# Optimization experiments

Hardware: AMD Instinct MI355X
Metric: run time of the kernel (lower is better)

Reference implementation:

```python
import jax, jax.numpy as jnp
import numpy as np

N = 100000
E = 1600000
IN, HID, OUT = 128, 32, 32


def gcn_conv(x, ei, ew, W, b, n):
    # PyG GCNConv: symmetric norm with self-loops, edge_attr as edge weight
    h = x @ W                                  # [n, d_out]
    row, col = ei[0], ei[1]
    loop = jnp.arange(n)
    row = jnp.concatenate([row, loop])
    col = jnp.concatenate([col, loop])
    ew = jnp.concatenate([ew, jnp.ones((n,), ew.dtype)])
    deg = jax.ops.segment_sum(ew, col, num_segments=n)
    dinv = jnp.where(deg > 0, jax.lax.rsqrt(deg), 0.0)
    norm = dinv[row] * ew * dinv[col]          # [E+n]
    out = jax.ops.segment_sum(norm[:, None] * h[row], col, num_segments=n)
    return out + b


def setup_inputs() -> dict:
    key = jax.random.key(0)
    ks = jax.random.split(key, 24)
    inp = {}
    for i in range(3):
        inp[f"x{i+1}"] = jax.random.normal(ks[i], (N, IN), jnp.float32)
        inp[f"ei{i+1}"] = jax.random.randint(ks[3 + i], (2, E), 0, N, jnp.int64)
        inp[f"ea{i+1}"] = jax.random.uniform(ks[6 + i], (E,), jnp.float32)
        inp[f"W{i+1}"] = jax.random.normal(ks[9 + i], (IN, HID), jnp.float32) * (IN ** -0.5)
        inp[f"b{i+1}"] = jnp.zeros((HID,), jnp.float32)
        inp[f"Wo{i+1}"] = jax.random.normal(ks[12 + i], (HID, OUT), jnp.float32) * (HID ** -0.5)
        inp[f"bo{i+1}"] = jnp.zeros((OUT,), jnp.float32)
    inp["att_w"] = jax.random.normal(ks[15], (HID, 1), jnp.float32) * (HID ** -0.5)
    return inp


def reference(x1, x2, x3, ei1, ei2, ei3, ea1, ea2, ea3,
              W1, W2, W3, b1, b2, b3,
              Wo1, Wo2, Wo3, bo1, bo2, bo3, att_w):
    xs = [x1, x2, x3]
    eis = [ei1, ei2, ei3]
    eas = [ea1, ea2, ea3]
    Ws = [W1, W2, W3]
    bs = [b1, b2, b3]
    Wos = [Wo1, Wo2, Wo3]
    bos = [bo1, bo2, bo3]

    embs, coefs = [], []
    for x, ei, ea, W, b in zip(xs, eis, eas, Ws, bs):
        e = jax.nn.relu(gcn_conv(x, ei, ea, W, b, N))   # [N, HID]; dropout is eval no-op
        embs.append(e)
        coefs.append(jnp.exp(jax.nn.leaky_relu(e @ att_w)))  # [N, 1]
    coef_sum = coefs[0] + coefs[1] + coefs[2]
    weights = [c / coef_sum for c in coefs]
    h = sum(w * e for w, e in zip(weights, embs))       # [N, HID]

    out = sum(gcn_conv(h, ei, ea, Wo, bo, N)
              for ei, ea, Wo, bo in zip(eis, eas, Wos, bos))
    return (out, weights[0], weights[1], weights[2])
```

## Files before the change

### kernel.cpp

```cpp
#include <hip/hip_runtime.h>
#include <hip/hip_fp16.h>

typedef unsigned short u16;
typedef unsigned int   u32;

#define N_NODES 100000
#define N_EDGES 1600000
#define IN_DIM  128
#define HID_DIM 32
#define OUT_DIM 32

#define BK   128
#define NBC  782
#define NBT  (3 * NBC)

#define PB    384
#define BINB  1024
#define CHUNK 12500
#define SC_N  (NBT * PB)
#define SC_CHUNK 2048
#define SC_G  ((SC_N + SC_CHUNK - 1) / SC_CHUNK)
#define CAP  3072
#define GN8  ((N_NODES * 8) / 256)


__global__ void binhist_kernel(const int* __restrict__ ei0, const int* __restrict__ ei1,
                               const int* __restrict__ ei2, int* __restrict__ hist_t) {
    __shared__ int hloc[NBT];
    for (int i = threadIdx.x; i < NBT; i += blockDim.x) hloc[i] = 0;
    __syncthreads();
    int b = blockIdx.x;
    int beg = b * CHUNK, end = beg + CHUNK;
    for (int e = beg + threadIdx.x; e < end; e += blockDim.x) {
        int c = (e >= 2 * N_EDGES) ? 2 : (e >= N_EDGES ? 1 : 0);
        const int* ei = (c == 0) ? ei0 : (c == 1) ? ei1 : ei2;
        int col = ei[N_EDGES + (e - c * N_EDGES)];
        atomicAdd(&hloc[c * NBC + (col >> 7)], 1);
    }
    __syncthreads();
    for (int g = threadIdx.x; g < NBT; g += blockDim.x)
        hist_t[g * PB + b] = hloc[g];
}


__global__ void scan1_kernel(const int* __restrict__ counts, int* __restrict__ rp1,
                             int* __restrict__ blocksum) {
    __shared__ int wsum[4];
    int tid = threadIdx.x;
    int base = blockIdx.x * SC_CHUNK + tid * 8;
    int vals[8];
    int tsum = 0;
    if (base < SC_N) {
        int4 v0 = *(const int4*)(counts + base);
        int4 v1 = *(const int4*)(counts + base + 4);
        vals[0] = v0.x; vals[1] = v0.y; vals[2] = v0.z; vals[3] = v0.w;
        vals[4] = v1.x; vals[5] = v1.y; vals[6] = v1.z; vals[7] = v1.w;
#pragma unroll
        for (int k = 0; k < 8; k++) tsum += vals[k];
    } else {
#pragma unroll
        for (int k = 0; k < 8; k++) vals[k] = 0;
    }
    int lane = tid & 63, wave = tid >> 6;
    int x = tsum;
    for (int d = 1; d < 64; d <<= 1) {
        int t = __shfl_up(x, d, 64);
        if (lane >= d) x += t;
    }
    if (lane == 63) wsum[wave] = x;
    __syncthreads();
    int woff = 0;
    for (int w = 0; w < wave; w++) woff += wsum[w];
    int run = woff + x - tsum;
    if (base < SC_N) {
#pragma unroll
        for (int k = 0; k < 8; k++) {
            run += vals[k];
            rp1[base + k + 1] = run;
        }
    }
    if (tid == blockDim.x - 1) blocksum[blockIdx.x] = woff + x;
}

__global__ void scan2_kernel(int* __restrict__ blocksum, int n) {
    __shared__ int wsum[4];
    int tid = threadIdx.x;
    int lane = tid & 63, wave = tid >> 6;
    int carry = 0;
    for (int base = 0; base < n; base += 256) {
        int i = base + tid;
        int v = (i < n) ? blocksum[i] : 0;
        int x = v;
        for (int d = 1; d < 64; d <<= 1) {
            int t = __shfl_up(x, d, 64);
            if (lane >= d) x += t;
        }
        if (lane == 63) wsum[wave] = x;
        __syncthreads();
        int woff = 0;
        for (int w = 0; w < wave; w++) woff += wsum[w];
        int total = wsum[0] + wsum[1] + wsum[2] + wsum[3];
        if (i < n) blocksum[i] = carry + woff + x - v;
        carry += total;
        __syncthreads();
    }
}

__global__ void scan3_kernel(int* __restrict__ rp1, const int* __restrict__ blocksum) {
    int i = blockIdx.x * blockDim.x + threadIdx.x;
    if (i < SC_N) rp1[i + 1] += blocksum[i / SC_CHUNK];
    if (i == 0) rp1[0] = 0;
}


__global__ void binscatter_kernel(const int* __restrict__ ei0, const int* __restrict__ ei1,
                                  const int* __restrict__ ei2,
                                  const float* __restrict__ ea0, const float* __restrict__ ea1,
                                  const float* __restrict__ ea2,
                                  const int* __restrict__ ofs, int2* __restrict__ stg) {
    __shared__ int base_l[NBT];
    int b = blockIdx.x;
    for (int g = threadIdx.x; g < NBT; g += blockDim.x) base_l[g] = ofs[g * PB + b];
    __syncthreads();
    int beg = b * CHUNK, end = beg + CHUNK;
    for (int e = beg + threadIdx.x; e < end; e += blockDim.x) {
        int c = (e >= 2 * N_EDGES) ? 2 : (e >= N_EDGES ? 1 : 0);
        int le = e - c * N_EDGES;
        const int* ei = (c == 0) ? ei0 : (c == 1) ? ei1 : ei2;
        const float* ea = (c == 0) ? ea0 : (c == 1) ? ea1 : ea2;
        int row = ei[le];
        int col = ei[N_EDGES + le];
        int g = c * NBC + (col >> 7);
        int slot = atomicAdd(&base_l[g], 1);
        stg[slot] = make_int2(row | ((col & 127) << 17), __float_as_int(ea[le]));
    }
}


__global__ void bucket_sort_kernel(int2* __restrict__ stg, const int* __restrict__ ofs,
                                   float* __restrict__ dinv, int* __restrict__ row_ptr) {
    __shared__ int2 buf[CAP];
    __shared__ int hist[BK];
    __shared__ float deg[BK];
    __shared__ float dl[BK];
    __shared__ int pref[BK];
    __shared__ int fill[BK];
    __shared__ int wtot;
    int tid = threadIdx.x;
    int g = blockIdx.x;
    int c = g / NBC;
    int colBase = (g % NBC) << 7;
    if (tid < BK) { hist[tid] = 0; deg[tid] = 1.0f; fill[tid] = 0; }
    __syncthreads();
    int beg = ofs[g * PB];
    int end = (g == NBT - 1) ? 3 * N_EDGES : ofs[(g + 1) * PB];
    int cnt = end - beg;
    if (cnt > CAP) cnt = CAP;
    for (int i = tid; i < cnt; i += blockDim.x) {
        int2 p = stg[beg + i];
        buf[i] = p;
        int cl = (p.x >> 17) & 127;
        atomicAdd(&hist[cl], 1);
        atomicAdd(&deg[cl], __int_as_float(p.y));
    }
    __syncthreads();
    int x = 0;
    if (tid < BK) {
        x = hist[tid];
        int lane = tid & 63;
        for (int d = 1; d < 64; d <<= 1) {
            int t = __shfl_up(x, d, 64);
            if (lane >= d) x += t;
        }
        if (tid == 63) wtot = x;
    }
    __syncthreads();
    if (tid < BK) {
        int incl = (tid >= 64) ? x + wtot : x;
        pref[tid] = incl - hist[tid];
        dl[tid] = rsqrtf(deg[tid]);
    }
    __syncthreads();
    for (int i = tid; i < cnt; i += blockDim.x) {
        int2 p = buf[i];
        int cl = (p.x >> 17) & 127;
        int r = atomicAdd(&fill[cl], 1);
        float v = __int_as_float(p.y) * dl[cl];
        stg[beg + pref[cl] + r] = make_int2(p.x, __float_as_int(v));
    }
    int col = colBase + tid;
    if (tid < BK && col < N_NODES) {
        dinv[(size_t)c * N_NODES + col] = dl[tid];
        row_ptr[(size_t)c * N_NODES + col] = beg + pref[tid];
    }
    if (g == NBT - 1 && tid == 0) row_ptr[3 * N_NODES] = 3 * N_EDGES;
}


__device__ inline u32 pack_half2(float a, float b) {
    __half2 h = __floats2half2_rn(a, b);
    union { __half2 h; u32 u; } cv; cv.h = h;
    return cv.u;
}

__device__ inline float2 unpack_half2(u32 u) {
    union { u32 u; __half2 h; } cv; cv.u = u;
    return __half22float2(cv.h);
}


__global__ void matmul_in3_kernel(const float* __restrict__ x0, const float* __restrict__ x1,
                                  const float* __restrict__ x2,
                                  const float* __restrict__ W0, const float* __restrict__ W1,
                                  const float* __restrict__ W2,
                                  const float* __restrict__ dinv,
                                  u16* __restrict__ h3) {
    __shared__ float Ws[IN_DIM * HID_DIM];
    int c = blockIdx.x / GN8;
    int lb = blockIdx.x % GN8;
    const float* x = (c == 0) ? x0 : (c == 1) ? x1 : x2;
    const float* W = (c == 0) ? W0 : (c == 1) ? W1 : W2;
    for (int i = threadIdx.x; i < IN_DIM * HID_DIM; i += blockDim.x) Ws[i] = W[i];
    __syncthreads();
    int gid = lb * blockDim.x + threadIdx.x;
    int v = gid >> 3;
    int t = gid & 7;
    const float* xr = x + (size_t)v * IN_DIM;
    float a0 = 0.f, a1 = 0.f, a2 = 0.f, a3 = 0.f;
#pragma unroll
    for (int j = 0; j < IN_DIM; j += 4) {
        float4 xv = *(const float4*)(xr + j);
        const float* wb = &Ws[j * HID_DIM + 4 * t];
        float4 w0 = *(const float4*)(wb);
        float4 w1 = *(const float4*)(wb + 32);
        float4 w2 = *(const float4*)(wb + 64);
        float4 w3 = *(const float4*)(wb + 96);
        a0 += xv.x * w0.x + xv.y * w1.x + xv.z * w2.x + xv.w * w3.x;
        a1 += xv.x * w0.y + xv.y * w1.y + xv.z * w2.y + xv.w * w3.y;
        a2 += xv.x * w0.z + xv.y * w1.z + xv.z * w2.z + xv.w * w3.z;
        a3 += xv.x * w0.w + xv.y * w1.w + xv.z * w2.w + xv.w * w3.w;
    }
    float s = dinv[(size_t)c * N_NODES + v];
    uint2 pk = make_uint2(pack_half2(a0 * s, a1 * s), pack_half2(a2 * s, a3 * s));
    *(uint2*)(h3 + ((size_t)c * N_NODES + v) * HID_DIM + 4 * t) = pk;
}


__global__ void matmul_hid3_kernel(const float* __restrict__ hmix,
                                   const float* __restrict__ Wo0, const float* __restrict__ Wo1,
                                   const float* __restrict__ Wo2,
                                   const float* __restrict__ dinv,
                                   u16* __restrict__ h23) {
    __shared__ float Ws[HID_DIM * OUT_DIM];
    int c = blockIdx.x / GN8;
    int lb = blockIdx.x % GN8;
    const float* Wo = (c == 0) ? Wo0 : (c == 1) ? Wo1 : Wo2;
    for (int i = threadIdx.x; i < HID_DIM * OUT_DIM; i += blockDim.x) Ws[i] = Wo[i];
    __syncthreads();
    int gid = lb * blockDim.x + threadIdx.x;
    int v = gid >> 3;
    int t = gid & 7;
    const float* hr = hmix + (size_t)v * HID_DIM;
    float a0 = 0.f, a1 = 0.f, a2 = 0.f, a3 = 0.f;
#pragma unroll
    for (int j = 0; j < HID_DIM; j += 4) {
        float4 hv = *(const float4*)(hr + j);
        const float* wb = &Ws[j * OUT_DIM + 4 * t];
        float4 w0 = *(const float4*)(wb);
        float4 w1 = *(const float4*)(wb + 32);
        float4 w2 = *(const float4*)(wb + 64);
        float4 w3 = *(const float4*)(wb + 96);
        a0 += hv.x * w0.x + hv.y * w1.x + hv.z * w2.x + hv.w * w3.x;
        a1 += hv.x * w0.y + hv.y * w1.y + hv.z * w2.y + hv.w * w3.y;
        a2 += hv.x * w0.z + hv.y * w1.z + hv.z * w2.z + hv.w * w3.z;
        a3 += hv.x * w0.w + hv.y * w1.w + hv.z * w2.w + hv.w * w3.w;
    }
    float s = dinv[(size_t)c * N_NODES + v];
    uint2 pk = make_uint2(pack_half2(a0 * s, a1 * s), pack_half2(a2 * s, a3 * s));
    *(uint2*)(h23 + ((size_t)c * N_NODES + v) * OUT_DIM + 4 * t) = pk;
}


__global__ void gather_combine_kernel(const int* __restrict__ row_ptr,
                                      const int2* __restrict__ csr,
                                      const u16* __restrict__ h3,
                                      const float* __restrict__ dinv,
                                      const float* __restrict__ b0,
                                      const float* __restrict__ b1,
                                      const float* __restrict__ b2,
                                      const float* __restrict__ att_w,
                                      float* __restrict__ hmix,
                                      float* __restrict__ wout) {
    int gid = blockIdx.x * blockDim.x + threadIdx.x;
    int v = gid >> 3;
    int t = gid & 7;
    float4 wv = *(const float4*)(att_w + t * 4);
    float e[3][4];
    float coef[3];
#pragma unroll
    for (int c = 0; c < 3; c++) {
        const u16* h = h3 + (size_t)c * N_NODES * HID_DIM;
        const float* bb = (c == 0) ? b0 : (c == 1) ? b1 : b2;
        int beg = row_ptr[c * N_NODES + v], end = row_ptr[c * N_NODES + v + 1];
        float a0 = 0.f, a1 = 0.f, a2 = 0.f, a3 = 0.f;
        for (int ee = beg; ee < end; ee++) {
            int2 p = csr[ee];
            int row = p.x & 0x1FFFF;
            float val = __int_as_float(p.y);
            uint2 u = *(const uint2*)(h + (size_t)row * HID_DIM + 4 * t);
            float2 f0 = unpack_half2(u.x);
            float2 f1 = unpack_half2(u.y);
            a0 += val * f0.x; a1 += val * f0.y; a2 += val * f1.x; a3 += val * f1.y;
        }
        float s = dinv[(size_t)c * N_NODES + v];
        uint2 u = *(const uint2*)(h + (size_t)v * HID_DIM + 4 * t);
        float2 f0 = unpack_half2(u.x);
        float2 f1 = unpack_half2(u.y);
        float4 bv = *(const float4*)(bb + t * 4);
        e[c][0] = fmaxf(a0 + s * f0.x + bv.x, 0.f);
        e[c][1] = fmaxf(a1 + s * f0.y + bv.y, 0.f);
        e[c][2] = fmaxf(a2 + s * f1.x + bv.z, 0.f);
        e[c][3] = fmaxf(a3 + s * f1.y + bv.w, 0.f);
        float dot = e[c][0] * wv.x + e[c][1] * wv.y + e[c][2] * wv.z + e[c][3] * wv.w;
        dot += __shfl_xor(dot, 1, 64);
        dot += __shfl_xor(dot, 2, 64);
        dot += __shfl_xor(dot, 4, 64);
        float lr = (dot > 0.0f) ? dot : 0.01f * dot;
        coef[c] = expf(lr);
    }
    float inv = 1.0f / (coef[0] + coef[1] + coef[2]);
    float w0 = coef[0] * inv, w1 = coef[1] * inv, w2 = coef[2] * inv;
    if (t == 0) {
        wout[v] = w0;
        wout[N_NODES + v] = w1;
        wout[2 * N_NODES + v] = w2;
    }
    float4 r;
    r.x = w0 * e[0][0] + w1 * e[1][0] + w2 * e[2][0];
    r.y = w0 * e[0][1] + w1 * e[1][1] + w2 * e[2][1];
    r.z = w0 * e[0][2] + w1 * e[1][2] + w2 * e[2][2];
    r.w = w0 * e[0][3] + w1 * e[1][3] + w2 * e[2][3];
    *(float4*)(hmix + (size_t)v * HID_DIM + t * 4) = r;
}


__global__ void gather_out_kernel(const int* __restrict__ row_ptr,
                                  const int2* __restrict__ csr,
                                  const u16* __restrict__ h23,
                                  const float* __restrict__ dinv,
                                  const float* __restrict__ bo0,
                                  const float* __restrict__ bo1,
                                  const float* __restrict__ bo2,
                                  float* __restrict__ out) {
    int gid = blockIdx.x * blockDim.x + threadIdx.x;
    int v = gid >> 3;
    int t = gid & 7;
    float4 b0 = *(const float4*)(bo0 + t * 4);
    float4 b1 = *(const float4*)(bo1 + t * 4);
    float4 b2 = *(const float4*)(bo2 + t * 4);
    float a0 = b0.x + b1.x + b2.x;
    float a1 = b0.y + b1.y + b2.y;
    float a2 = b0.z + b1.z + b2.z;
    float a3 = b0.w + b1.w + b2.w;
#pragma unroll
    for (int c = 0; c < 3; c++) {
        const u16* h2 = h23 + (size_t)c * N_NODES * OUT_DIM;
        int beg = row_ptr[c * N_NODES + v], end = row_ptr[c * N_NODES + v + 1];
        for (int ee = beg; ee < end; ee++) {
            int2 p = csr[ee];
            int row = p.x & 0x1FFFF;
            float val = __int_as_float(p.y);
            uint2 u = *(const uint2*)(h2 + (size_t)row * OUT_DIM + 4 * t);
            float2 f0 = unpack_half2(u.x);
            float2 f1 = unpack_half2(u.y);
            a0 += val * f0.x; a1 += val * f0.y; a2 += val * f1.x; a3 += val * f1.y;
        }
        float s = dinv[(size_t)c * N_NODES + v];
        uint2 u = *(const uint2*)(h2 + (size_t)v * OUT_DIM + 4 * t);
        float2 f0 = unpack_half2(u.x);
        float2 f1 = unpack_half2(u.y);
        a0 += s * f0.x; a1 += s * f0.y; a2 += s * f1.x; a3 += s * f1.y;
    }
    float4 ov; ov.x = a0; ov.y = a1; ov.z = a2; ov.w = a3;
    *(float4*)(out + (size_t)v * OUT_DIM + t * 4) = ov;
}


extern "C" void kernel_launch(void* const* d_in, const int* in_sizes, int n_in,
                              void* d_out, int out_size, void* d_ws, size_t ws_size,
                              hipStream_t stream) {
    const float* x[3];  const int* ei[3];  const float* ea[3];
    const float* W[3];  const float* b[3]; const float* Wo[3]; const float* bo[3];
    for (int c = 0; c < 3; c++) {
        x[c]  = (const float*)d_in[7 * c + 0];
        ei[c] = (const int*)  d_in[7 * c + 1];
        ea[c] = (const float*)d_in[7 * c + 2];
        W[c]  = (const float*)d_in[7 * c + 3];
        b[c]  = (const float*)d_in[7 * c + 4];
        Wo[c] = (const float*)d_in[7 * c + 5];
        bo[c] = (const float*)d_in[7 * c + 6];
    }
    const float* att_w = (const float*)d_in[21];
    float* out = (float*)d_out;
    float* wout = out + (size_t)N_NODES * OUT_DIM;

    int*   wsb      = (int*)d_ws;
    float* dinv     = (float*)wsb;
    int*   row_ptr  = wsb + 3 * N_NODES;
    int*   blocksum = row_ptr + 3 * N_NODES + 4;
    size_t stg_off  = (size_t)(3 * N_NODES + 3 * N_NODES + 4 + 512);
    stg_off = (stg_off + 3) & ~(size_t)3;
    int2*  stg      = (int2*)(wsb + stg_off);
    u16*   hA       = (u16*)(stg + 3 * (size_t)N_EDGES);
    int*   hist_t   = (int*)hA;
    int*   ofs      = hist_t + SC_N;
    float* hmix     = (float*)(hA + 3 * (size_t)N_NODES * HID_DIM);

    const int B = 256;

    binhist_kernel<<<PB, BINB, 0, stream>>>(ei[0], ei[1], ei[2], hist_t);
    scan1_kernel<<<SC_G, B, 0, stream>>>(hist_t, ofs, blocksum);
    scan2_kernel<<<1, B, 0, stream>>>(blocksum, SC_G);
    scan3_kernel<<<(SC_N + B - 1) / B, B, 0, stream>>>(ofs, blocksum);
    binscatter_kernel<<<PB, BINB, 0, stream>>>(ei[0], ei[1], ei[2], ea[0], ea[1], ea[2],
                                               ofs, stg);
    bucket_sort_kernel<<<NBT, B, 0, stream>>>(stg, ofs, dinv, row_ptr);

    matmul_in3_kernel<<<3 * GN8, B, 0, stream>>>(x[0], x[1], x[2], W[0], W[1], W[2],
                                                 dinv, hA);
    gather_combine_kernel<<<GN8, B, 0, stream>>>(row_ptr, stg, hA, dinv,
                                                 b[0], b[1], b[2], att_w, hmix, wout);

    matmul_hid3_kernel<<<3 * GN8, B, 0, stream>>>(hmix, Wo[0], Wo[1], Wo[2], dinv, hA);
    gather_out_kernel<<<GN8, B, 0, stream>>>(row_ptr, stg, hA, dinv,
                                             bo[0], bo[1], bo[2], out);
}
```

Measured before the change: 687.6 us.

## Pack CSR entries into 32 bits, widen gather threads, drop scan3 pass

Bucket sort now writes a separate 4-byte CSR entry per edge holding the 17-bit row index and a 15-bit half-precision normalized weight (sign bit dropped), instead of an 8-byte int2. This halves the index traffic in both gather kernels. The gather kernels switch from 8 to 4 threads per node, each loading 16-byte half vectors, which cuts shuffle steps and redundant CSR reads. The scan3 fixup kernel is removed: block carries are added on the fly wherever offsets are read, and the binning partition count changes from 384 to 256 blocks. The cost is reduced edge-weight precision and fewer threads in flight for the gathers.

```diff
diff --git a/kernel.cpp b/kernel.cpp
--- a/kernel.cpp
+++ b/kernel.cpp
@@ -14,14 +14,19 @@
 #define NBC  782
 #define NBT  (3 * NBC)
 
-#define PB    384
+#define PB    256
 #define BINB  1024
-#define CHUNK 12500
+#define CHUNK 18750
 #define SC_N  (NBT * PB)
 #define SC_CHUNK 2048
 #define SC_G  ((SC_N + SC_CHUNK - 1) / SC_CHUNK)
 #define CAP  3072
 #define GN8  ((N_NODES * 8) / 256)
+#define GN4  ((N_NODES * 4 + 255) / 256)
+
+__device__ inline int ofs_at(const int* __restrict__ rp1, const int* __restrict__ bs, int m) {
+    return m ? rp1[m] + bs[(m - 1) >> 11] : 0;
+}
 
 
 __global__ void binhist_kernel(const int* __restrict__ ei0, const int* __restrict__ ei1,
@@ -80,6 +85,7 @@
         }
     }
     if (tid == blockDim.x - 1) blocksum[blockIdx.x] = woff + x;
+    if (blockIdx.x == 0 && tid == 0) rp1[0] = 0;
 }
 
 __global__ void scan2_kernel(int* __restrict__ blocksum, int n) {
@@ -106,21 +112,17 @@
     }
 }
 
-__global__ void scan3_kernel(int* __restrict__ rp1, const int* __restrict__ blocksum) {
-    int i = blockIdx.x * blockDim.x + threadIdx.x;
-    if (i < SC_N) rp1[i + 1] += blocksum[i / SC_CHUNK];
-    if (i == 0) rp1[0] = 0;
-}
-
 
 __global__ void binscatter_kernel(const int* __restrict__ ei0, const int* __restrict__ ei1,
                                   const int* __restrict__ ei2,
                                   const float* __restrict__ ea0, const float* __restrict__ ea1,
                                   const float* __restrict__ ea2,
-                                  const int* __restrict__ ofs, int2* __restrict__ stg) {
+                                  const int* __restrict__ rp1, const int* __restrict__ bsum,
+                                  int2* __restrict__ stg) {
     __shared__ int base_l[NBT];
     int b = blockIdx.x;
-    for (int g = threadIdx.x; g < NBT; g += blockDim.x) base_l[g] = ofs[g * PB + b];
+    for (int g = threadIdx.x; g < NBT; g += blockDim.x)
+        base_l[g] = ofs_at(rp1, bsum, g * PB + b);
     __syncthreads();
     int beg = b * CHUNK, end = beg + CHUNK;
     for (int e = beg + threadIdx.x; e < end; e += blockDim.x) {
@@ -137,7 +139,9 @@
 }
 
 
-__global__ void bucket_sort_kernel(int2* __restrict__ stg, const int* __restrict__ ofs,
+__global__ void bucket_sort_kernel(const int2* __restrict__ stg, const int* __restrict__ rp1,
+                                   const int* __restrict__ bsum,
+                                   u32* __restrict__ csr,
                                    float* __restrict__ dinv, int* __restrict__ row_ptr) {
     __shared__ int2 buf[CAP];
     __shared__ int hist[BK];
@@ -152,8 +156,8 @@
     int colBase = (g % NBC) << 7;
     if (tid < BK) { hist[tid] = 0; deg[tid] = 1.0f; fill[tid] = 0; }
     __syncthreads();
-    int beg = ofs[g * PB];
-    int end = (g == NBT - 1) ? 3 * N_EDGES : ofs[(g + 1) * PB];
+    int beg = ofs_at(rp1, bsum, g * PB);
+    int end = (g == NBT - 1) ? 3 * N_EDGES : ofs_at(rp1, bsum, (g + 1) * PB);
     int cnt = end - beg;
     if (cnt > CAP) cnt = CAP;
     for (int i = tid; i < cnt; i += blockDim.x) {
@@ -186,7 +190,9 @@
         int cl = (p.x >> 17) & 127;
         int r = atomicAdd(&fill[cl], 1);
         float v = __int_as_float(p.y) * dl[cl];
-        stg[beg + pref[cl] + r] = make_int2(p.x, __float_as_int(v));
+        __half h = __float2half(v);
+        u32 hb = (u32)(*(u16*)&h) & 0x7FFF;
+        csr[beg + pref[cl] + r] = (u32)(p.x & 0x1FFFF) | (hb << 17);
     }
     int col = colBase + tid;
     if (tid < BK && col < N_NODES) {
@@ -206,6 +212,10 @@
 __device__ inline float2 unpack_half2(u32 u) {
     union { u32 u; __half2 h; } cv; cv.u = u;
     return __half22float2(cv.h);
+}
+
+__device__ inline float val15(u32 meta) {
+    return unpack_half2(meta >> 17).x;
 }
 
 
@@ -282,7 +292,7 @@
 
 
 __global__ void gather_combine_kernel(const int* __restrict__ row_ptr,
-                                      const int2* __restrict__ csr,
+                                      const u32* __restrict__ csr,
                                       const u16* __restrict__ h3,
                                       const float* __restrict__ dinv,
                                       const float* __restrict__ b0,
@@ -292,39 +302,49 @@
                                       float* __restrict__ hmix,
                                       float* __restrict__ wout) {
     int gid = blockIdx.x * blockDim.x + threadIdx.x;
-    int v = gid >> 3;
-    int t = gid & 7;
-    float4 wv = *(const float4*)(att_w + t * 4);
-    float e[3][4];
+    int v = gid >> 2;
+    int t = gid & 3;
+    if (v >= N_NODES) return;
+    float4 wv0 = *(const float4*)(att_w + t * 8);
+    float4 wv1 = *(const float4*)(att_w + t * 8 + 4);
+    float e[3][8];
     float coef[3];
 #pragma unroll
     for (int c = 0; c < 3; c++) {
         const u16* h = h3 + (size_t)c * N_NODES * HID_DIM;
         const float* bb = (c == 0) ? b0 : (c == 1) ? b1 : b2;
         int beg = row_ptr[c * N_NODES + v], end = row_ptr[c * N_NODES + v + 1];
-        float a0 = 0.f, a1 = 0.f, a2 = 0.f, a3 = 0.f;
+        float a[8];
+#pragma unroll
+        for (int k = 0; k < 8; k++) a[k] = 0.f;
         for (int ee = beg; ee < end; ee++) {
-            int2 p = csr[ee];
-            int row = p.x & 0x1FFFF;
-            float val = __int_as_float(p.y);
-            uint2 u = *(const uint2*)(h + (size_t)row * HID_DIM + 4 * t);
-            float2 f0 = unpack_half2(u.x);
-            float2 f1 = unpack_half2(u.y);
-            a0 += val * f0.x; a1 += val * f0.y; a2 += val * f1.x; a3 += val * f1.y;
+            u32 m = csr[ee];
+            int row = m & 0x1FFFF;
+            float val = val15(m);
+            uint4 u = *(const uint4*)(h + (size_t)row * HID_DIM + 8 * t);
+            float2 f0 = unpack_half2(u.x), f1 = unpack_half2(u.y);
+            float2 f2 = unpack_half2(u.z), f3 = unpack_half2(u.w);
+            a[0] += val * f0.x; a[1] += val * f0.y; a[2] += val * f1.x; a[3] += val * f1.y;
+            a[4] += val * f2.x; a[5] += val * f2.y; a[6] += val * f3.x; a[7] += val * f3.y;
         }
         float s = dinv[(size_t)c * N_NODES + v];
-        uint2 u = *(const uint2*)(h + (size_t)v * HID_DIM + 4 * t);
-        float2 f0 = unpack_half2(u.x);
-        float2 f1 = unpack_half2(u.y);
-        float4 bv = *(const float4*)(bb + t * 4);
-        e[c][0] = fmaxf(a0 + s * f0.x + bv.x, 0.f);
-        e[c][1] = fmaxf(a1 + s * f0.y + bv.y, 0.f);
-        e[c][2] = fmaxf(a2 + s * f1.x + bv.z, 0.f);
-        e[c][3] = fmaxf(a3 + s * f1.y + bv.w, 0.f);
-        float dot = e[c][0] * wv.x + e[c][1] * wv.y + e[c][2] * wv.z + e[c][3] * wv.w;
+        uint4 u = *(const uint4*)(h + (size_t)v * HID_DIM + 8 * t);
+        float2 f0 = unpack_half2(u.x), f1 = unpack_half2(u.y);
+        float2 f2 = unpack_half2(u.z), f3 = unpack_half2(u.w);
+        float4 bv0 = *(const float4*)(bb + t * 8);
+        float4 bv1 = *(const float4*)(bb + t * 8 + 4);
+        e[c][0] = fmaxf(a[0] + s * f0.x + bv0.x, 0.f);
+        e[c][1] = fmaxf(a[1] + s * f0.y + bv0.y, 0.f);
+        e[c][2] = fmaxf(a[2] + s * f1.x + bv0.z, 0.f);
+        e[c][3] = fmaxf(a[3] + s * f1.y + bv0.w, 0.f);
+        e[c][4] = fmaxf(a[4] + s * f2.x + bv1.x, 0.f);
+        e[c][5] = fmaxf(a[5] + s * f2.y + bv1.y, 0.f);
+        e[c][6] = fmaxf(a[6] + s * f3.x + bv1.z, 0.f);
+        e[c][7] = fmaxf(a[7] + s * f3.y + bv1.w, 0.f);
+        float dot = e[c][0] * wv0.x + e[c][1] * wv0.y + e[c][2] * wv0.z + e[c][3] * wv0.w
+                  + e[c][4] * wv1.x + e[c][5] * wv1.y + e[c][6] * wv1.z + e[c][7] * wv1.w;
         dot += __shfl_xor(dot, 1, 64);
         dot += __shfl_xor(dot, 2, 64);
-        dot += __shfl_xor(dot, 4, 64);
         float lr = (dot > 0.0f) ? dot : 0.01f * dot;
         coef[c] = expf(lr);
     }
@@ -335,17 +355,22 @@
         wout[N_NODES + v] = w1;
         wout[2 * N_NODES + v] = w2;
     }
-    float4 r;
-    r.x = w0 * e[0][0] + w1 * e[1][0] + w2 * e[2][0];
-    r.y = w0 * e[0][1] + w1 * e[1][1] + w2 * e[2][1];
-    r.z = w0 * e[0][2] + w1 * e[1][2] + w2 * e[2][2];
-    r.w = w0 * e[0][3] + w1 * e[1][3] + w2 * e[2][3];
-    *(float4*)(hmix + (size_t)v * HID_DIM + t * 4) = r;
+    float4 r0, r1;
+    r0.x = w0 * e[0][0] + w1 * e[1][0] + w2 * e[2][0];
+    r0.y = w0 * e[0][1] + w1 * e[1][1] + w2 * e[2][1];
+    r0.z = w0 * e[0][2] + w1 * e[1][2] + w2 * e[2][2];
+    r0.w = w0 * e[0][3] + w1 * e[1][3] + w2 * e[2][3];
+    r1.x = w0 * e[0][4] + w1 * e[1][4] + w2 * e[2][4];
+    r1.y = w0 * e[0][5] + w1 * e[1][5] + w2 * e[2][5];
+    r1.z = w0 * e[0][6] + w1 * e[1][6] + w2 * e[2][6];
+    r1.w = w0 * e[0][7] + w1 * e[1][7] + w2 * e[2][7];
+    *(float4*)(hmix + (size_t)v * HID_DIM + t * 8) = r0;
+    *(float4*)(hmix + (size_t)v * HID_DIM + t * 8 + 4) = r1;
 }
 
 
 __global__ void gather_out_kernel(const int* __restrict__ row_ptr,
-                                  const int2* __restrict__ csr,
+                                  const u32* __restrict__ csr,
                                   const u16* __restrict__ h23,
                                   const float* __restrict__ dinv,
                                   const float* __restrict__ bo0,
@@ -353,36 +378,46 @@
                                   const float* __restrict__ bo2,
                                   float* __restrict__ out) {
     int gid = blockIdx.x * blockDim.x + threadIdx.x;
-    int v = gid >> 3;
-    int t = gid & 7;
-    float4 b0 = *(const float4*)(bo0 + t * 4);
-    float4 b1 = *(const float4*)(bo1 + t * 4);
-    float4 b2 = *(const float4*)(bo2 + t * 4);
-    float a0 = b0.x + b1.x + b2.x;
-    float a1 = b0.y + b1.y + b2.y;
-    float a2 = b0.z + b1.z + b2.z;
-    float a3 = b0.w + b1.w + b2.w;
+    int v = gid >> 2;
+    int t = gid & 3;
+    if (v >= N_NODES) return;
+    float4 p0 = *(const float4*)(bo0 + t * 8);
+    float4 p1 = *(const float4*)(bo0 + t * 8 + 4);
+    float4 q0 = *(const float4*)(bo1 + t * 8);
+    float4 q1 = *(const float4*)(bo1 + t * 8 + 4);
+    float4 s0 = *(const float4*)(bo2 + t * 8);
+    float4 s1 = *(const float4*)(bo2 + t * 8 + 4);
+    float a[8];
+    a[0] = p0.x + q0.x + s0.x; a[1] = p0.y + q0.y + s0.y;
+    a[2] = p0.z + q0.z + s0.z; a[3] = p0.w + q0.w + s0.w;
+    a[4] = p1.x + q1.x + s1.x; a[5] = p1.y + q1.y + s1.y;
+    a[6] = p1.z + q1.z + s1.z; a[7] = p1.w + q1.w + s1.w;
 #pragma unroll
     for (int c = 0; c < 3; c++) {
         const u16* h2 = h23 + (size_t)c * N_NODES * OUT_DIM;
         int beg = row_ptr[c * N_NODES + v], end = row_ptr[c * N_NODES + v + 1];
         for (int ee = beg; ee < end; ee++) {
-            int2 p = csr[ee];
-            int row = p.x & 0x1FFFF;
-            float val = __int_as_float(p.y);
-            uint2 u = *(const uint2*)(h2 + (size_t)row * OUT_DIM + 4 * t);
-            float2 f0 = unpack_half2(u.x);
-            float2 f1 = unpack_half2(u.y);
-            a0 += val * f0.x; a1 += val * f0.y; a2 += val * f1.x; a3 += val * f1.y;
+            u32 m = csr[ee];
+            int row = m & 0x1FFFF;
+            float val = val15(m);
+            uint4 u = *(const uint4*)(h2 + (size_t)row * OUT_DIM + 8 * t);
+            float2 f0 = unpack_half2(u.x), f1 = unpack_half2(u.y);
+            float2 f2 = unpack_half2(u.z), f3 = unpack_half2(u.w);
+            a[0] += val * f0.x; a[1] += val * f0.y; a[2] += val * f1.x; a[3] += val * f1.y;
+            a[4] += val * f2.x; a[5] += val * f2.y; a[6] += val * f3.x; a[7] += val * f3.y;
         }
         float s = dinv[(size_t)c * N_NODES + v];
-        uint2 u = *(const uint2*)(h2 + (size_t)v * OUT_DIM + 4 * t);
-        float2 f0 = unpack_half2(u.x);
-        float2 f1 = unpack_half2(u.y);
-        a0 += s * f0.x; a1 += s * f0.y; a2 += s * f1.x; a3 += s * f1.y;
-    }
-    float4 ov; ov.x = a0; ov.y = a1; ov.z = a2; ov.w = a3;
-    *(float4*)(out + (size_t)v * OUT_DIM + t * 4) = ov;
+        uint4 u = *(const uint4*)(h2 + (size_t)v * OUT_DIM + 8 * t);
+        float2 f0 = unpack_half2(u.x), f1 = unpack_half2(u.y);
+        float2 f2 = unpack_half2(u.z), f3 = unpack_half2(u.w);
+        a[0] += s * f0.x; a[1] += s * f0.y; a[2] += s * f1.x; a[3] += s * f1.y;
+        a[4] += s * f2.x; a[5] += s * f2.y; a[6] += s * f3.x; a[7] += s * f3.y;
+    }
+    float4 o0, o1;
+    o0.x = a[0]; o0.y = a[1]; o0.z = a[2]; o0.w = a[3];
+    o1.x = a[4]; o1.y = a[5]; o1.z = a[6]; o1.w = a[7];
+    *(float4*)(out + (size_t)v * OUT_DIM + t * 8) = o0;
+    *(float4*)(out + (size_t)v * OUT_DIM + t * 8 + 4) = o1;
 }
 
 
@@ -411,27 +446,27 @@
     size_t stg_off  = (size_t)(3 * N_NODES + 3 * N_NODES + 4 + 512);
     stg_off = (stg_off + 3) & ~(size_t)3;
     int2*  stg      = (int2*)(wsb + stg_off);
-    u16*   hA       = (u16*)(stg + 3 * (size_t)N_EDGES);
+    u32*   csr      = (u32*)(stg + 3 * (size_t)N_EDGES);
+    u16*   hA       = (u16*)(csr + 3 * (size_t)N_EDGES);
     int*   hist_t   = (int*)hA;
-    int*   ofs      = hist_t + SC_N;
+    int*   rp1      = hist_t + SC_N;
     float* hmix     = (float*)(hA + 3 * (size_t)N_NODES * HID_DIM);
 
     const int B = 256;
 
     binhist_kernel<<<PB, BINB, 0, stream>>>(ei[0], ei[1], ei[2], hist_t);
-    scan1_kernel<<<SC_G, B, 0, stream>>>(hist_t, ofs, blocksum);
+    scan1_kernel<<<SC_G, B, 0, stream>>>(hist_t, rp1, blocksum);
     scan2_kernel<<<1, B, 0, stream>>>(blocksum, SC_G);
-    scan3_kernel<<<(SC_N + B - 1) / B, B, 0, stream>>>(ofs, blocksum);
     binscatter_kernel<<<PB, BINB, 0, stream>>>(ei[0], ei[1], ei[2], ea[0], ea[1], ea[2],
-                                               ofs, stg);
-    bucket_sort_kernel<<<NBT, B, 0, stream>>>(stg, ofs, dinv, row_ptr);
+                                               rp1, blocksum, stg);
+    bucket_sort_kernel<<<NBT, B, 0, stream>>>(stg, rp1, blocksum, csr, dinv, row_ptr);
 
     matmul_in3_kernel<<<3 * GN8, B, 0, stream>>>(x[0], x[1], x[2], W[0], W[1], W[2],
                                                  dinv, hA);
-    gather_combine_kernel<<<GN8, B, 0, stream>>>(row_ptr, stg, hA, dinv,
+    gather_combine_kernel<<<GN4, B, 0, stream>>>(row_ptr, csr, hA, dinv,
                                                  b[0], b[1], b[2], att_w, hmix, wout);
 
     matmul_hid3_kernel<<<3 * GN8, B, 0, stream>>>(hmix, Wo[0], Wo[1], Wo[2], dinv, hA);
-    gather_out_kernel<<<GN8, B, 0, stream>>>(row_ptr, stg, hA, dinv,
+    gather_out_kernel<<<GN4, B, 0, stream>>>(row_ptr, csr, hA, dinv,
                                              bo[0], bo[1], bo[2], out);
 }
```

After: 610.6 us. 1.13x faster.
